# Kernel tuning notes

Measured on AMD Instinct MI355X. Metric: run time of the kernel, lower is better.

The kernel has to match this reference:

```python
import jax, jax.numpy as jnp
import numpy as np

INPUT_SIZE = 1024
HIDDEN_SIZE = 1024
B, L = 32, 2048


def setup_inputs() -> dict:
    key = jax.random.key(0)
    k_h, k_m, k_lw, k_vw, k_vq = jax.random.split(key, 5)
    h = jax.random.normal(k_h, (B, L, INPUT_SIZE), dtype=jnp.float32)
    mask = jax.random.randint(k_m, (B, L), 0, 2).astype(bool)
    # nn.Linear(input+hidden, hidden): weight (hidden, input+hidden), bias (hidden,)
    fan = INPUT_SIZE + HIDDEN_SIZE + HIDDEN_SIZE
    ln_w = jax.random.uniform(k_lw, (HIDDEN_SIZE, INPUT_SIZE + HIDDEN_SIZE),
                              minval=-1.0, maxval=1.0, dtype=jnp.float32) * np.sqrt(6.0 / fan)
    ln_b = jnp.zeros((HIDDEN_SIZE,), dtype=jnp.float32)
    # v: Linear(hidden, 1, bias=False) -> weight (1, hidden); store as (hidden,)
    v_w = jax.random.uniform(k_vw, (HIDDEN_SIZE,), minval=-1.0, maxval=1.0,
                             dtype=jnp.float32) * np.sqrt(6.0 / (HIDDEN_SIZE + 1))
    vq = jax.random.uniform(k_vq, (HIDDEN_SIZE,), dtype=jnp.float32)
    return {"h": h, "mask": mask, "ln_w": ln_w, "ln_b": ln_b, "v_w": v_w, "vq": vq}


def reference(h, mask, ln_w, ln_b, v_w, vq):
    # ln(cat([h, vq], -1)) == h @ W_h^T + vq @ W_vq^T + b  (vq is constant over b,l)
    W_h = ln_w[:, :INPUT_SIZE]          # (H, I)
    W_vq = ln_w[:, INPUT_SIZE:]         # (H, H)
    bias = ln_b + W_vq @ vq             # (H,)
    pre = jnp.einsum('bli,hi->blh', h, W_h) + bias  # (B, L, H)
    s = jnp.tanh(pre) @ v_w             # (B, L)
    s = s - (~mask).astype(s.dtype) * 10000.0
    a = jax.nn.softmax(s, axis=1)       # softmax over seq dim
    r = jnp.einsum('bl,bli->bi', a, h)  # (B, I)
    return r  # dropout omitted (eval mode)
```

## Files before the change

kernel.cpp:

```cpp
#include <hip/hip_runtime.h>
#include <hip/hip_bf16.h>

typedef short  bf16x8s __attribute__((ext_vector_type(8)));
typedef float  f32x4   __attribute__((ext_vector_type(4)));

#define BATCH 32
#define SEQL  2048
#define NROWS (BATCH * SEQL)
#define IN    1024
#define HID   1024

#define BM 128
#define BN 128
#define BK 32

__device__ __forceinline__ unsigned int pack2bf(float f0, float f1) {
    unsigned int u0 = __float_as_uint(f0) + 0x8000u;
    unsigned int u1 = __float_as_uint(f1) + 0x8000u;
    return __builtin_amdgcn_perm(u1, u0, 0x07060302u);
}

__device__ __forceinline__ float tanh_fast(float x) {
    float xc = fminf(fmaxf(x, -15.f), 15.f);
    float t  = __builtin_amdgcn_exp2f(xc * 2.8853900817779268f);
    return (t - 1.f) * __builtin_amdgcn_rcpf(t + 1.f);
}

__global__ __launch_bounds__(256) void convw_kernel(const float* __restrict__ ln_w,
                                                    unsigned short* __restrict__ whb) {
    const int n = blockIdx.x;
    const int t = threadIdx.x;
    float4 v = ((const float4*)(ln_w + (size_t)n * 2048))[t];
    uint2 pk;
    pk.x = pack2bf(v.x, v.y);
    pk.y = pack2bf(v.z, v.w);
    *(uint2*)(whb + (size_t)n * 1024 + t * 4) = pk;
}

__global__ __launch_bounds__(256) void bias_kernel(const float* __restrict__ ln_w,
                                                   const float* __restrict__ ln_b,
                                                   const float* __restrict__ vq,
                                                   float* __restrict__ bias) {
    const int wave = threadIdx.x >> 6;
    const int lane = threadIdx.x & 63;
    const int n = blockIdx.x * 4 + wave;
    const float* wrow = ln_w + (size_t)n * 2048 + 1024;
    float sum = 0.f;
    #pragma unroll
    for (int j = 0; j < 16; ++j) {
        int k = lane + j * 64;
        sum += wrow[k] * vq[k];
    }
    #pragma unroll
    for (int off = 32; off; off >>= 1) sum += __shfl_xor(sum, off);
    if (lane == 0) bias[n] = ln_b[n] + sum;
}

__global__ __launch_bounds__(256) void gemm_tanh_kernel(const float* __restrict__ hmat,
                                                        const unsigned short* __restrict__ whb,
                                                        const float* __restrict__ bias,
                                                        const float* __restrict__ vw,
                                                        float* __restrict__ s_buf) {
    __shared__ __align__(16) unsigned short As[BM * BK];
    __shared__ __align__(16) unsigned short Bs[BN * BK];

    const int tid  = threadIdx.x;
    const int cb   = blockIdx.x & 7;
    const int rb   = blockIdx.x >> 3;
    const int wave = tid >> 6;
    const int lane = tid & 63;
    const int quad = lane >> 4;
    const int l15  = lane & 15;
    const int wy   = wave >> 1;
    const int wx   = wave & 1;
    const int row0 = rb * BM;
    const int col0 = cb * BN;

    const int srow = tid >> 2;
    const int sg   = tid & 3;
    const int swz  = (srow >> 1) & 3;
    const float*          gA0 = hmat + (size_t)(row0 + srow)      * 1024 + sg * 8;
    const float*          gA1 = hmat + (size_t)(row0 + srow + 64) * 1024 + sg * 8;
    const unsigned short* gB0 = whb  + (size_t)(col0 + srow)      * 1024 + sg * 8;
    const unsigned short* gB1 = gB0 + (size_t)64 * 1024;
    unsigned short* wA0 = As + srow * 32 + ((sg ^ swz) * 8);
    unsigned short* wA1 = wA0 + 64 * 32;
    unsigned short* wB0 = Bs + srow * 32 + ((sg ^ swz) * 8);
    unsigned short* wB1 = wB0 + 64 * 32;

    const unsigned short* rA[4];
    const unsigned short* rB[4];
    #pragma unroll
    for (int i = 0; i < 4; ++i) {
        int ra = wy * 64 + i * 16 + l15;
        rA[i] = As + ra * 32 + ((quad ^ ((ra >> 1) & 3)) * 8);
        int rn = wx * 64 + i * 16 + l15;
        rB[i] = Bs + rn * 32 + ((quad ^ ((rn >> 1) & 3)) * 8);
    }

    f32x4 acc[4][4];
    #pragma unroll
    for (int i = 0; i < 4; ++i)
        #pragma unroll
        for (int j = 0; j < 4; ++j)
            acc[i][j] = (f32x4){0.f, 0.f, 0.f, 0.f};

    for (int k0 = 0; k0 < 1024; k0 += BK) {
        float4 va0 = *(const float4*)(gA0 + k0);
        float4 va1 = *(const float4*)(gA0 + k0 + 4);
        float4 va2 = *(const float4*)(gA1 + k0);
        float4 va3 = *(const float4*)(gA1 + k0 + 4);
        uint4  vb0 = *(const uint4*)(gB0 + k0);
        uint4  vb1 = *(const uint4*)(gB1 + k0);

        __syncthreads();

        uint4 pa0, pa1;
        pa0.x = pack2bf(va0.x, va0.y); pa0.y = pack2bf(va0.z, va0.w);
        pa0.z = pack2bf(va1.x, va1.y); pa0.w = pack2bf(va1.z, va1.w);
        pa1.x = pack2bf(va2.x, va2.y); pa1.y = pack2bf(va2.z, va2.w);
        pa1.z = pack2bf(va3.x, va3.y); pa1.w = pack2bf(va3.z, va3.w);
        *(uint4*)wA0 = pa0;
        *(uint4*)wA1 = pa1;
        *(uint4*)wB0 = vb0;
        *(uint4*)wB1 = vb1;

        __syncthreads();

        bf16x8s af[4], bfv[4];
        #pragma unroll
        for (int i = 0; i < 4; ++i) af[i]  = *(const bf16x8s*)rA[i];
        #pragma unroll
        for (int i = 0; i < 4; ++i) bfv[i] = *(const bf16x8s*)rB[i];
        #pragma unroll
        for (int mt = 0; mt < 4; ++mt)
            #pragma unroll
            for (int nt = 0; nt < 4; ++nt)
                acc[mt][nt] = __builtin_amdgcn_mfma_f32_16x16x32_bf16(af[mt], bfv[nt], acc[mt][nt], 0, 0, 0);
    }

    const int colb = col0 + wx * 64 + l15;
    float vwv[4], bv[4];
    #pragma unroll
    for (int nt = 0; nt < 4; ++nt) {
        vwv[nt] = vw[colb + nt * 16];
        bv[nt]  = bias[colb + nt * 16];
    }
    const int rowb = row0 + wy * 64 + quad * 4;
    #pragma unroll
    for (int mt = 0; mt < 4; ++mt) {
        #pragma unroll
        for (int r = 0; r < 4; ++r) {
            float p = 0.f;
            #pragma unroll
            for (int nt = 0; nt < 4; ++nt)
                p += tanh_fast(acc[mt][nt][r] + bv[nt]) * vwv[nt];
            p += __shfl_xor(p, 1);
            p += __shfl_xor(p, 2);
            p += __shfl_xor(p, 4);
            p += __shfl_xor(p, 8);
            if (l15 == 0) atomicAdd(&s_buf[rowb + mt * 16 + r], p);
        }
    }
}

__global__ __launch_bounds__(256) void softmax_kernel(const float* __restrict__ s_buf,
                                                      const int* __restrict__ mask,
                                                      float* __restrict__ a_buf) {
    const int b    = blockIdx.x;
    const int t    = threadIdx.x;
    const int wave = t >> 6;
    const int lane = t & 63;
    __shared__ float redm[4];
    __shared__ float reds[4];
    float sv[8];
    float mx = -3.0e38f;
    #pragma unroll
    for (int j = 0; j < 8; ++j) {
        int l = t + j * 256;
        float v = s_buf[b * 2048 + l];
        if (mask[b * 2048 + l] == 0) v -= 10000.f;
        sv[j] = v;
        mx = fmaxf(mx, v);
    }
    #pragma unroll
    for (int off = 32; off; off >>= 1) mx = fmaxf(mx, __shfl_xor(mx, off));
    if (lane == 0) redm[wave] = mx;
    __syncthreads();
    mx = fmaxf(fmaxf(redm[0], redm[1]), fmaxf(redm[2], redm[3]));
    float sum = 0.f;
    #pragma unroll
    for (int j = 0; j < 8; ++j) {
        sv[j] = __expf(sv[j] - mx);
        sum += sv[j];
    }
    #pragma unroll
    for (int off = 32; off; off >>= 1) sum += __shfl_xor(sum, off);
    if (lane == 0) reds[wave] = sum;
    __syncthreads();
    sum = reds[0] + reds[1] + reds[2] + reds[3];
    float inv = 1.f / sum;
    #pragma unroll
    for (int j = 0; j < 8; ++j)
        a_buf[b * 2048 + t + j * 256] = sv[j] * inv;
}

__global__ __launch_bounds__(256) void r_kernel(const float* __restrict__ hmat,
                                                const float* __restrict__ a_buf,
                                                float* __restrict__ out) {
    const int b  = blockIdx.x >> 4;
    const int lc = blockIdx.x & 15;
    const int t  = threadIdx.x;
    __shared__ float aw[128];
    if (t < 128) aw[t] = a_buf[b * 2048 + lc * 128 + t];
    __syncthreads();
    const float4* hp = (const float4*)hmat + (size_t)(b * 2048 + lc * 128) * 256;
    float ax = 0.f, ay = 0.f, az = 0.f, aq = 0.f;
    #pragma unroll 4
    for (int l = 0; l < 128; ++l) {
        float4 hv = hp[(size_t)l * 256 + t];
        float av = aw[l];
        ax += av * hv.x; ay += av * hv.y; az += av * hv.z; aq += av * hv.w;
    }
    float* op = out + b * 1024 + t * 4;
    atomicAdd(op + 0, ax);
    atomicAdd(op + 1, ay);
    atomicAdd(op + 2, az);
    atomicAdd(op + 3, aq);
}

extern "C" void kernel_launch(void* const* d_in, const int* in_sizes, int n_in,
                              void* d_out, int out_size, void* d_ws, size_t ws_size,
                              hipStream_t stream) {
    const float* h    = (const float*)d_in[0];
    const int*   mask = (const int*)d_in[1];
    const float* ln_w = (const float*)d_in[2];
    const float* ln_b = (const float*)d_in[3];
    const float* v_w  = (const float*)d_in[4];
    const float* vq   = (const float*)d_in[5];
    float* out = (float*)d_out;

    char* ws = (char*)d_ws;
    unsigned short* whb  = (unsigned short*)ws;
    float* bias          = (float*)(ws + 2097152);
    float* s_buf         = (float*)(ws + 2097152 + 4096);
    float* a_buf         = (float*)(ws + 2097152 + 4096 + 262144);

    hipMemsetAsync(s_buf, 0, NROWS * sizeof(float), stream);
    hipMemsetAsync(d_out, 0, (size_t)out_size * sizeof(float), stream);

    convw_kernel<<<1024, 256, 0, stream>>>(ln_w, whb);
    bias_kernel<<<256, 256, 0, stream>>>(ln_w, ln_b, vq, bias);
    gemm_tanh_kernel<<<(NROWS / BM) * (HID / BN), 256, 0, stream>>>(h, whb, bias, v_w, s_buf);
    softmax_kernel<<<BATCH, 256, 0, stream>>>(s_buf, mask, a_buf);
    r_kernel<<<BATCH * 16, 256, 0, stream>>>(h, a_buf, out);
}
```

Before: 633.0 us.

## Pre-convert h to bf16, use direct global-to-LDS loads, remap blocks by XCD

Adds a pass that converts h to bf16 in workspace when space allows, so the GEMM can load both operands with global_load_lds straight into LDS (pre-swizzled source addresses) instead of loading fp32 and packing in registers. Fuses the weight conversion and bias kernels into one prep kernel, remaps block indices so blocks sharing row tiles land on the same XCD for L2 reuse, and doubles the r_kernel grid with shorter sequence chunks. The extra conversion pass costs a full read of h plus a bf16 write, and the fp32 fallback path stays in place if the workspace is too small.

After: 608.5 us. 1.04x faster.

```diff
diff --git a/kernel.cpp b/kernel.cpp
--- a/kernel.cpp
+++ b/kernel.cpp
@@ -14,6 +14,13 @@
 #define BN 128
 #define BK 32
 
+#define WHB_OFF   0u
+#define BIAS_OFF  0x200000u
+#define SBUF_OFF  0x210000u
+#define ABUF_OFF  0x250000u
+#define HB_OFF    0x290000u
+#define WS_NEED_BF16 ((size_t)HB_OFF + (size_t)NROWS * IN * 2)
+
 __device__ __forceinline__ unsigned int pack2bf(float f0, float f1) {
     unsigned int u0 = __float_as_uint(f0) + 0x8000u;
     unsigned int u1 = __float_as_uint(f1) + 0x8000u;
@@ -26,37 +33,60 @@
     return (t - 1.f) * __builtin_amdgcn_rcpf(t + 1.f);
 }
 
-__global__ __launch_bounds__(256) void convw_kernel(const float* __restrict__ ln_w,
-                                                    unsigned short* __restrict__ whb) {
+__device__ __forceinline__ void gl2lds16(const void* g, void* l) {
+    __builtin_amdgcn_global_load_lds(
+        (const __attribute__((address_space(1))) unsigned int*)g,
+        (__attribute__((address_space(3))) unsigned int*)l, 16, 0, 0);
+}
+
+__device__ __forceinline__ void block_map(int bi, int& rb, int& cb) {
+    int xcd  = bi & 7;
+    int slot = bi >> 3;
+    rb = xcd + 8 * (slot >> 3);
+    cb = slot & 7;
+}
+
+__global__ __launch_bounds__(256) void prep_kernel(const float* __restrict__ ln_w,
+                                                   const float* __restrict__ ln_b,
+                                                   const float* __restrict__ vq,
+                                                   unsigned short* __restrict__ whb,
+                                                   float* __restrict__ bias) {
     const int n = blockIdx.x;
     const int t = threadIdx.x;
+    const int wave = t >> 6;
+    const int lane = t & 63;
     float4 v = ((const float4*)(ln_w + (size_t)n * 2048))[t];
     uint2 pk;
     pk.x = pack2bf(v.x, v.y);
     pk.y = pack2bf(v.z, v.w);
     *(uint2*)(whb + (size_t)n * 1024 + t * 4) = pk;
-}
-
-__global__ __launch_bounds__(256) void bias_kernel(const float* __restrict__ ln_w,
-                                                   const float* __restrict__ ln_b,
-                                                   const float* __restrict__ vq,
-                                                   float* __restrict__ bias) {
-    const int wave = threadIdx.x >> 6;
-    const int lane = threadIdx.x & 63;
-    const int n = blockIdx.x * 4 + wave;
     const float* wrow = ln_w + (size_t)n * 2048 + 1024;
-    float sum = 0.f;
-    #pragma unroll
-    for (int j = 0; j < 16; ++j) {
-        int k = lane + j * 64;
-        sum += wrow[k] * vq[k];
-    }
-    #pragma unroll
-    for (int off = 32; off; off >>= 1) sum += __shfl_xor(sum, off);
-    if (lane == 0) bias[n] = ln_b[n] + sum;
-}
-
-__global__ __launch_bounds__(256) void gemm_tanh_kernel(const float* __restrict__ hmat,
+    float s = 0.f;
+    #pragma unroll
+    for (int j = 0; j < 4; ++j) {
+        int k = t + j * 256;
+        s += wrow[k] * vq[k];
+    }
+    #pragma unroll
+    for (int off = 32; off; off >>= 1) s += __shfl_xor(s, off);
+    __shared__ float red[4];
+    if (lane == 0) red[wave] = s;
+    __syncthreads();
+    if (t == 0) bias[n] = ln_b[n] + red[0] + red[1] + red[2] + red[3];
+}
+
+__global__ __launch_bounds__(256) void convh_kernel(const float* __restrict__ h,
+                                                    unsigned short* __restrict__ hb) {
+    size_t idx = ((size_t)blockIdx.x * 256 + threadIdx.x) * 8;
+    float4 a = *(const float4*)(h + idx);
+    float4 b = *(const float4*)(h + idx + 4);
+    uint4 p;
+    p.x = pack2bf(a.x, a.y); p.y = pack2bf(a.z, a.w);
+    p.z = pack2bf(b.x, b.y); p.w = pack2bf(b.z, b.w);
+    *(uint4*)(hb + idx) = p;
+}
+
+__global__ __launch_bounds__(256) void gemm_bf16_kernel(const unsigned short* __restrict__ hb,
                                                         const unsigned short* __restrict__ whb,
                                                         const float* __restrict__ bias,
                                                         const float* __restrict__ vw,
@@ -64,9 +94,9 @@
     __shared__ __align__(16) unsigned short As[BM * BK];
     __shared__ __align__(16) unsigned short Bs[BN * BK];
 
-    const int tid  = threadIdx.x;
-    const int cb   = blockIdx.x & 7;
-    const int rb   = blockIdx.x >> 3;
+    const int tid = threadIdx.x;
+    int rb, cb;
+    block_map(blockIdx.x, rb, cb);
     const int wave = tid >> 6;
     const int lane = tid & 63;
     const int quad = lane >> 4;
@@ -79,14 +109,14 @@
     const int srow = tid >> 2;
     const int sg   = tid & 3;
     const int swz  = (srow >> 1) & 3;
-    const float*          gA0 = hmat + (size_t)(row0 + srow)      * 1024 + sg * 8;
-    const float*          gA1 = hmat + (size_t)(row0 + srow + 64) * 1024 + sg * 8;
-    const unsigned short* gB0 = whb  + (size_t)(col0 + srow)      * 1024 + sg * 8;
+    const unsigned short* gA0 = hb  + (size_t)(row0 + srow) * 1024 + ((sg ^ swz) * 8);
+    const unsigned short* gA1 = gA0 + (size_t)64 * 1024;
+    const unsigned short* gB0 = whb + (size_t)(col0 + srow) * 1024 + ((sg ^ swz) * 8);
     const unsigned short* gB1 = gB0 + (size_t)64 * 1024;
-    unsigned short* wA0 = As + srow * 32 + ((sg ^ swz) * 8);
-    unsigned short* wA1 = wA0 + 64 * 32;
-    unsigned short* wB0 = Bs + srow * 32 + ((sg ^ swz) * 8);
-    unsigned short* wB1 = wB0 + 64 * 32;
+    unsigned short* lA0 = As + tid * 8;
+    unsigned short* lA1 = As + 2048 + tid * 8;
+    unsigned short* lB0 = Bs + tid * 8;
+    unsigned short* lB1 = Bs + 2048 + tid * 8;
 
     const unsigned short* rA[4];
     const unsigned short* rB[4];
@@ -106,25 +136,11 @@
             acc[i][j] = (f32x4){0.f, 0.f, 0.f, 0.f};
 
     for (int k0 = 0; k0 < 1024; k0 += BK) {
-        float4 va0 = *(const float4*)(gA0 + k0);
-        float4 va1 = *(const float4*)(gA0 + k0 + 4);
-        float4 va2 = *(const float4*)(gA1 + k0);
-        float4 va3 = *(const float4*)(gA1 + k0 + 4);
-        uint4  vb0 = *(const uint4*)(gB0 + k0);
-        uint4  vb1 = *(const uint4*)(gB1 + k0);
-
         __syncthreads();
-
-        uint4 pa0, pa1;
-        pa0.x = pack2bf(va0.x, va0.y); pa0.y = pack2bf(va0.z, va0.w);
-        pa0.z = pack2bf(va1.x, va1.y); pa0.w = pack2bf(va1.z, va1.w);
-        pa1.x = pack2bf(va2.x, va2.y); pa1.y = pack2bf(va2.z, va2.w);
-        pa1.z = pack2bf(va3.x, va3.y); pa1.w = pack2bf(va3.z, va3.w);
-        *(uint4*)wA0 = pa0;
-        *(uint4*)wA1 = pa1;
-        *(uint4*)wB0 = vb0;
-        *(uint4*)wB1 = vb1;
-
+        gl2lds16(gA0 + k0, lA0);
+        gl2lds16(gA1 + k0, lA1);
+        gl2lds16(gB0 + k0, lB0);
+        gl2lds16(gB1 + k0, lB1);
         __syncthreads();
 
         bf16x8s af[4], bfv[4];
@@ -164,6 +180,112 @@
     }
 }
 
+__global__ __launch_bounds__(256) void gemm_tanh_kernel(const float* __restrict__ hmat,
+                                                        const unsigned short* __restrict__ whb,
+                                                        const float* __restrict__ bias,
+                                                        const float* __restrict__ vw,
+                                                        float* __restrict__ s_buf) {
+    __shared__ __align__(16) unsigned short As[BM * BK];
+    __shared__ __align__(16) unsigned short Bs[BN * BK];
+
+    const int tid = threadIdx.x;
+    int rb, cb;
+    block_map(blockIdx.x, rb, cb);
+    const int wave = tid >> 6;
+    const int lane = tid & 63;
+    const int quad = lane >> 4;
+    const int l15  = lane & 15;
+    const int wy   = wave >> 1;
+    const int wx   = wave & 1;
+    const int row0 = rb * BM;
+    const int col0 = cb * BN;
+
+    const int srow = tid >> 2;
+    const int sg   = tid & 3;
+    const int swz  = (srow >> 1) & 3;
+    const float*          gA0 = hmat + (size_t)(row0 + srow)      * 1024 + sg * 8;
+    const float*          gA1 = hmat + (size_t)(row0 + srow + 64) * 1024 + sg * 8;
+    const unsigned short* gB0 = whb  + (size_t)(col0 + srow)      * 1024 + ((sg ^ swz) * 8);
+    const unsigned short* gB1 = gB0 + (size_t)64 * 1024;
+    unsigned short* wA0 = As + srow * 32 + ((sg ^ swz) * 8);
+    unsigned short* wA1 = wA0 + 64 * 32;
+    unsigned short* lB0 = Bs + tid * 8;
+    unsigned short* lB1 = Bs + 2048 + tid * 8;
+
+    const unsigned short* rA[4];
+    const unsigned short* rB[4];
+    #pragma unroll
+    for (int i = 0; i < 4; ++i) {
+        int ra = wy * 64 + i * 16 + l15;
+        rA[i] = As + ra * 32 + ((quad ^ ((ra >> 1) & 3)) * 8);
+        int rn = wx * 64 + i * 16 + l15;
+        rB[i] = Bs + rn * 32 + ((quad ^ ((rn >> 1) & 3)) * 8);
+    }
+
+    f32x4 acc[4][4];
+    #pragma unroll
+    for (int i = 0; i < 4; ++i)
+        #pragma unroll
+        for (int j = 0; j < 4; ++j)
+            acc[i][j] = (f32x4){0.f, 0.f, 0.f, 0.f};
+
+    for (int k0 = 0; k0 < 1024; k0 += BK) {
+        float4 va0 = *(const float4*)(gA0 + k0);
+        float4 va1 = *(const float4*)(gA0 + k0 + 4);
+        float4 va2 = *(const float4*)(gA1 + k0);
+        float4 va3 = *(const float4*)(gA1 + k0 + 4);
+
+        __syncthreads();
+        gl2lds16(gB0 + k0, lB0);
+        gl2lds16(gB1 + k0, lB1);
+
+        uint4 pa0, pa1;
+        pa0.x = pack2bf(va0.x, va0.y); pa0.y = pack2bf(va0.z, va0.w);
+        pa0.z = pack2bf(va1.x, va1.y); pa0.w = pack2bf(va1.z, va1.w);
+        pa1.x = pack2bf(va2.x, va2.y); pa1.y = pack2bf(va2.z, va2.w);
+        pa1.z = pack2bf(va3.x, va3.y); pa1.w = pack2bf(va3.z, va3.w);
+        *(uint4*)wA0 = pa0;
+        *(uint4*)wA1 = pa1;
+
+        __syncthreads();
+
+        bf16x8s af[4], bfv[4];
+        #pragma unroll
+        for (int i = 0; i < 4; ++i) af[i]  = *(const bf16x8s*)rA[i];
+        #pragma unroll
+        for (int i = 0; i < 4; ++i) bfv[i] = *(const bf16x8s*)rB[i];
+        #pragma unroll
+        for (int mt = 0; mt < 4; ++mt)
+            #pragma unroll
+            for (int nt = 0; nt < 4; ++nt)
+                acc[mt][nt] = __builtin_amdgcn_mfma_f32_16x16x32_bf16(af[mt], bfv[nt], acc[mt][nt], 0, 0, 0);
+    }
+
+    const int colb = col0 + wx * 64 + l15;
+    float vwv[4], bv[4];
+    #pragma unroll
+    for (int nt = 0; nt < 4; ++nt) {
+        vwv[nt] = vw[colb + nt * 16];
+        bv[nt]  = bias[colb + nt * 16];
+    }
+    const int rowb = row0 + wy * 64 + quad * 4;
+    #pragma unroll
+    for (int mt = 0; mt < 4; ++mt) {
+        #pragma unroll
+        for (int r = 0; r < 4; ++r) {
+            float p = 0.f;
+            #pragma unroll
+            for (int nt = 0; nt < 4; ++nt)
+                p += tanh_fast(acc[mt][nt][r] + bv[nt]) * vwv[nt];
+            p += __shfl_xor(p, 1);
+            p += __shfl_xor(p, 2);
+            p += __shfl_xor(p, 4);
+            p += __shfl_xor(p, 8);
+            if (l15 == 0) atomicAdd(&s_buf[rowb + mt * 16 + r], p);
+        }
+    }
+}
+
 __global__ __launch_bounds__(256) void softmax_kernel(const float* __restrict__ s_buf,
                                                       const int* __restrict__ mask,
                                                       float* __restrict__ a_buf) {
@@ -208,16 +330,16 @@
 __global__ __launch_bounds__(256) void r_kernel(const float* __restrict__ hmat,
                                                 const float* __restrict__ a_buf,
                                                 float* __restrict__ out) {
-    const int b  = blockIdx.x >> 4;
-    const int lc = blockIdx.x & 15;
+    const int b  = blockIdx.x >> 5;
+    const int lc = blockIdx.x & 31;
     const int t  = threadIdx.x;
-    __shared__ float aw[128];
-    if (t < 128) aw[t] = a_buf[b * 2048 + lc * 128 + t];
+    __shared__ float aw[64];
+    if (t < 64) aw[t] = a_buf[b * 2048 + lc * 64 + t];
     __syncthreads();
-    const float4* hp = (const float4*)hmat + (size_t)(b * 2048 + lc * 128) * 256;
+    const float4* hp = (const float4*)hmat + (size_t)(b * 2048 + lc * 64) * 256;
     float ax = 0.f, ay = 0.f, az = 0.f, aq = 0.f;
-    #pragma unroll 4
-    for (int l = 0; l < 128; ++l) {
+    #pragma unroll 8
+    for (int l = 0; l < 64; ++l) {
         float4 hv = hp[(size_t)l * 256 + t];
         float av = aw[l];
         ax += av * hv.x; ay += av * hv.y; az += av * hv.z; aq += av * hv.w;
@@ -241,17 +363,24 @@
     float* out = (float*)d_out;
 
     char* ws = (char*)d_ws;
-    unsigned short* whb  = (unsigned short*)ws;
-    float* bias          = (float*)(ws + 2097152);
-    float* s_buf         = (float*)(ws + 2097152 + 4096);
-    float* a_buf         = (float*)(ws + 2097152 + 4096 + 262144);
+    unsigned short* whb = (unsigned short*)(ws + WHB_OFF);
+    float* bias         = (float*)(ws + BIAS_OFF);
+    float* s_buf        = (float*)(ws + SBUF_OFF);
+    float* a_buf        = (float*)(ws + ABUF_OFF);
+    unsigned short* hb  = (unsigned short*)(ws + HB_OFF);
+
+    const bool use_bf16_h = (ws_size >= WS_NEED_BF16);
 
     hipMemsetAsync(s_buf, 0, NROWS * sizeof(float), stream);
     hipMemsetAsync(d_out, 0, (size_t)out_size * sizeof(float), stream);
 
-    convw_kernel<<<1024, 256, 0, stream>>>(ln_w, whb);
-    bias_kernel<<<256, 256, 0, stream>>>(ln_w, ln_b, vq, bias);
-    gemm_tanh_kernel<<<(NROWS / BM) * (HID / BN), 256, 0, stream>>>(h, whb, bias, v_w, s_buf);
+    prep_kernel<<<1024, 256, 0, stream>>>(ln_w, ln_b, vq, whb, bias);
+    if (use_bf16_h) {
+        convh_kernel<<<32768, 256, 0, stream>>>(h, hb);
+        gemm_bf16_kernel<<<(NROWS / BM) * (HID / BN), 256, 0, stream>>>(hb, whb, bias, v_w, s_buf);
+    } else {
+        gemm_tanh_kernel<<<(NROWS / BM) * (HID / BN), 256, 0, stream>>>(h, whb, bias, v_w, s_buf);
+    }
     softmax_kernel<<<BATCH, 256, 0, stream>>>(s_buf, mask, a_buf);
-    r_kernel<<<BATCH * 16, 256, 0, stream>>>(h, a_buf, out);
-}
+    r_kernel<<<BATCH * 32, 256, 0, stream>>>(h, a_buf, out);
+}
```
